# Performance work log

Measured on AMD Instinct MI355X. Metric: run time of the kernel, lower is better.

## Reference

```python
import jax, jax.numpy as jnp
import numpy as np

B, NE, NS, NI, NIS, H, NL = 8192, 210, 7, 8, 2, 128, 3


def setup_inputs() -> dict:
    key = jax.random.key(0)
    ks = jax.random.split(key, 24)
    inp = {}
    inp["F_dist"] = jax.random.normal(ks[0], (B, 45), jnp.float32)
    inp["F_cos"] = jax.random.normal(ks[1], (B, NE), jnp.float32)
    inp["F_sin"] = jax.random.normal(ks[2], (B, NE), jnp.float32)
    inp["F_angle"] = jax.random.normal(ks[3], (B, 8), jnp.float32)
    # Zscore tables: row 0 = mean, row 1 = std (kept away from zero)
    def zscore(k, f):
        k1, k2 = jax.random.split(k)
        mean = jax.random.normal(k1, (1, f), jnp.float32)
        std = jax.random.uniform(k2, (1, f), jnp.float32, 0.5, 1.5)
        return jnp.concatenate([mean, std], axis=0)
    inp["Zscore_dist"] = zscore(ks[4], 45)
    inp["Zscore_cos"] = zscore(ks[5], NE)
    inp["Zscore_sin"] = zscore(ks[6], NE)
    # per-expert index tables
    inp["INDEX3_4BD"] = jax.random.randint(ks[7], (NE, 6), 0, 45, jnp.int32)
    inp["INDEX5"] = jax.random.randint(ks[8], (NS,), 0, NE, jnp.int32)
    # 210 experts: Linear(8,H) + (NL-1)x Linear(H,H) + Linear(H,1), all tanh-separated
    s = 0.1
    inp["W1"] = jax.random.normal(ks[9], (NE, NI, H), jnp.float32) * s
    inp["b1"] = jax.random.normal(ks[10], (NE, H), jnp.float32) * s
    inp["Wh"] = jax.random.normal(ks[11], (NL - 1, NE, H, H), jnp.float32) * s
    inp["bh"] = jax.random.normal(ks[12], (NL - 1, NE, H), jnp.float32) * s
    inp["Wo"] = jax.random.normal(ks[13], (NE, H, 1), jnp.float32) * s
    inp["bo"] = jax.random.normal(ks[14], (NE, 1), jnp.float32) * s
    # 7 small experts: Linear(2,H) + (NL-1)x Linear(H,H) + Linear(H,1)
    inp["W1s"] = jax.random.normal(ks[15], (NS, NIS, H), jnp.float32) * s
    inp["b1s"] = jax.random.normal(ks[16], (NS, H), jnp.float32) * s
    inp["Whs"] = jax.random.normal(ks[17], (NL - 1, NS, H, H), jnp.float32) * s
    inp["bhs"] = jax.random.normal(ks[18], (NL - 1, NS, H), jnp.float32) * s
    inp["Wos"] = jax.random.normal(ks[19], (NS, H, 1), jnp.float32) * s
    inp["bos"] = jax.random.normal(ks[20], (NS, 1), jnp.float32) * s
    return inp


def _expert_stack(F, W1, b1, Wh, bh, Wo, bo):
    # F: [B, E, ni] -> [B, E, 1]; grouped tiny MLPs with tanh
    h = jnp.tanh(jnp.einsum("bei,eih->beh", F, W1) + b1)
    for l in range(Wh.shape[0]):
        h = jnp.tanh(jnp.einsum("beh,ehg->beg", h, Wh[l]) + bh[l])
    return jnp.einsum("beh,eho->beo", h, Wo) + bo


def reference(F_dist, F_cos, F_sin, F_angle, Zscore_dist, Zscore_cos, Zscore_sin,
              INDEX3_4BD, INDEX5,
              W1, b1, Wh, bh, Wo, bo, W1s, b1s, Whs, bhs, Wos, bos):
    FNorm_dist = (F_dist - Zscore_dist[0]) / Zscore_dist[1]  # [B,45]
    FNorm_cos = (F_cos - Zscore_cos[0]) / Zscore_cos[1]      # [B,210]
    FNorm_sin = (F_sin - Zscore_sin[0]) / Zscore_sin[1]      # [B,210]
    # gather per-expert 6 dist features + own cos/sin -> [B,210,8]
    Fd = FNorm_dist[:, INDEX3_4BD]                            # [B,210,6]
    F = jnp.concatenate([Fd, FNorm_cos[:, :, None], FNorm_sin[:, :, None]], axis=-1)
    out = _expert_stack(F, W1, b1, Wh, bh, Wo, bo)            # [B,210,1]
    total = jnp.sum(out, axis=1)                              # [B,1]
    # 7 small experts on (cos, sin) pairs picked by INDEX5
    Fs = jnp.stack([FNorm_cos[:, INDEX5], FNorm_sin[:, INDEX5]], axis=-1)  # [B,7,2]
    outs = _expert_stack(Fs, W1s, b1s, Whs, bhs, Wos, bos)    # [B,7,1]
    total = total + jnp.sum(outs, axis=1)
    return total
```

## Files before the change

### kernel.cpp

```cpp
#include <hip/hip_runtime.h>
#include <hip/hip_bf16.h>
#include <stdint.h>

#define NB 8192
#define NE 210
#define NS 7
#define NEXP 217
#define NI 8
#define H 128
#define BT 256
#define NTILE (NB / BT)
#define BLOB_STRIDE 71680
#define BIAS_OFF 4096
#define WH0_OFF 6144
#define WH1_OFF 38912
#define SMEM_BYTES 67584

#define O_BLOB 0u
#define O_F    16000000u
#define O_FS   43525120u
#define O_PART 43754496u

typedef __attribute__((ext_vector_type(8))) short bf16x8;
typedef __attribute__((ext_vector_type(4))) float f32x4;
typedef __attribute__((ext_vector_type(16))) float f32x16;
typedef __attribute__((ext_vector_type(2))) int i32x2;

union I4V { int4 i; bf16x8 v; unsigned u[4]; };
union C16 { f32x16 v; f32x4 q[4]; };

__device__ __forceinline__ unsigned short f2bf(float f) {
  unsigned u = __float_as_uint(f);
  u += 0x7fffu + ((u >> 16) & 1u);
  return (unsigned short)(u >> 16);
}
__device__ __forceinline__ float fast_tanh(float x) {
  float e = __builtin_amdgcn_exp2f(2.8853900817779268f * x);
  return 1.0f - 2.0f * __builtin_amdgcn_rcpf(1.0f + e);
}
__device__ __forceinline__ unsigned pk_bf16(float a, float b) {
  unsigned r;
  asm("v_cvt_pk_bf16_f32 %0, %1, %2" : "=v"(r) : "v"(a), "v"(b));
  return r;
}
__device__ __forceinline__ void glds16(const void* g, void* l) {
  __builtin_amdgcn_global_load_lds(
      (const __attribute__((address_space(1))) unsigned int*)g,
      (__attribute__((address_space(3))) unsigned int*)l, 16, 0, 0);
}

__device__ __forceinline__ void transition(const f32x16 (&acc)[4], bf16x8 (&bn)[8]) {
#pragma unroll
  for (int kk = 0; kk < 8; ++kk) {
    const int ms = kk >> 1, ko = (kk & 1) * 8;
    unsigned P0 = pk_bf16(fast_tanh(acc[ms][ko + 0]), fast_tanh(acc[ms][ko + 1]));
    unsigned P1 = pk_bf16(fast_tanh(acc[ms][ko + 2]), fast_tanh(acc[ms][ko + 3]));
    unsigned P2 = pk_bf16(fast_tanh(acc[ms][ko + 4]), fast_tanh(acc[ms][ko + 5]));
    unsigned P3 = pk_bf16(fast_tanh(acc[ms][ko + 6]), fast_tanh(acc[ms][ko + 7]));
    i32x2 s0 = __builtin_amdgcn_permlane32_swap((int)P0, (int)P2, false, false);
    i32x2 s1 = __builtin_amdgcn_permlane32_swap((int)P1, (int)P3, false, false);
    I4V r;
    r.u[0] = (unsigned)s0.x;
    r.u[1] = (unsigned)s1.x;
    r.u[2] = (unsigned)s0.y;
    r.u[3] = (unsigned)s1.y;
    bn[kk] = r.v;
  }
}

__device__ __forceinline__ void hidden_layer(f32x16 (&acc)[4], const bf16x8 (&bn)[8],
                                             const uint8_t* wb, const float* biaL,
                                             int row, int hi, int hi4) {
  {
    int soff0 = (hi ^ (row & 15)) << 4;
#pragma unroll
    for (int mt = 0; mt < 4; ++mt) {
      bf16x8 aF = *(const bf16x8*)(wb + (mt * 32 + row) * 256 + soff0);
      C16 c0;
#pragma unroll
      for (int i = 0; i < 4; ++i)
        c0.q[i] = *(const f32x4*)(biaL + mt * 32 + i * 8 + hi4);
      acc[mt] = __builtin_amdgcn_mfma_f32_32x32x16_bf16(aF, bn[0], c0.v, 0, 0, 0);
    }
  }
#pragma unroll
  for (int kk = 1; kk < 8; ++kk) {
    int soff = ((2 * kk + hi) ^ (row & 15)) << 4;
#pragma unroll
    for (int mt = 0; mt < 4; ++mt) {
      bf16x8 aF = *(const bf16x8*)(wb + (mt * 32 + row) * 256 + soff);
      acc[mt] = __builtin_amdgcn_mfma_f32_32x32x16_bf16(aF, bn[kk], acc[mt], 0, 0, 0);
    }
  }
}

__global__ __launch_bounds__(128) void k_pack(
    const float* __restrict__ W1, const float* __restrict__ Wh,
    const float* __restrict__ W1s, const float* __restrict__ Whs,
    const float* __restrict__ bh, const float* __restrict__ bhs,
    const float* __restrict__ Wo, const float* __restrict__ Wos,
    const float* __restrict__ bo, const float* __restrict__ bos,
    uint8_t* __restrict__ blob) {
  int bid = blockIdx.x;
  int e = bid / 3, sec = bid % 3;
  int n = threadIdx.x;
  uint8_t* be = blob + (size_t)e * BLOB_STRIDE;
  bool big = e < NE;
  int s = e - NE;
  if (sec == 0) {
    union { int4 v[2]; unsigned short u[16]; } row;
    row.v[0] = make_int4(0, 0, 0, 0);
    row.v[1] = make_int4(0, 0, 0, 0);
    if (big) {
      for (int k = 0; k < NI; ++k) row.u[k] = f2bf(W1[((size_t)e * NI + k) * H + n]);
    } else {
      for (int k = 0; k < 2; ++k) row.u[k] = f2bf(W1s[((size_t)s * 2 + k) * H + n]);
    }
    *(int4*)(be + n * 32) = row.v[0];
    *(int4*)(be + n * 32 + 16) = row.v[1];
    float* bsec = (float*)(be + BIAS_OFF);
    bsec[n]       = big ? bh[(size_t)e * H + n]          : bhs[(size_t)s * H + n];
    bsec[128 + n] = big ? bh[((size_t)NE + e) * H + n]   : bhs[((size_t)NS + s) * H + n];
    bsec[256 + n] = big ? Wo[(size_t)e * H + n]          : Wos[(size_t)s * H + n];
    if (n == 0) bsec[384] = big ? bo[e] : bos[s];
  } else {
    int l = sec - 1;
    union { int4 v[16]; unsigned short u[128]; } row;
    if (big) {
      for (int k = 0; k < H; ++k)
        row.u[k] = f2bf(Wh[(((size_t)l * NE + e) * H + k) * H + n]);
    } else {
      for (int k = 0; k < H; ++k)
        row.u[k] = f2bf(Whs[(((size_t)l * NS + s) * H + k) * H + n]);
    }
    int4* dst = (int4*)(be + (l ? WH1_OFF : WH0_OFF) + n * 256);
    for (int c = 0; c < 16; ++c) dst[c] = row.v[c ^ (n & 15)];
  }
}

__global__ __launch_bounds__(256) void k_fbuild(
    const float* __restrict__ F_dist, const float* __restrict__ F_cos,
    const float* __restrict__ F_sin,
    const float* __restrict__ Zd, const float* __restrict__ Zc,
    const float* __restrict__ Zs,
    const int* __restrict__ IDX3, const int* __restrict__ IDX5,
    uint16_t* __restrict__ F, uint16_t* __restrict__ Fs) {
  int bid = blockIdx.x;
  int e = bid >> 5, tile = bid & 31;
  int b = tile * 256 + threadIdx.x;
  if (e < NE) {
    float cv = (F_cos[(size_t)b * NE + e] - Zc[e]) / Zc[NE + e];
    float sv = (F_sin[(size_t)b * NE + e] - Zs[e]) / Zs[NE + e];
    union { int4 v; unsigned short u[8]; } o;
    for (int j = 0; j < 6; ++j) {
      int id = IDX3[e * 6 + j];
      float x = (F_dist[(size_t)b * 45 + id] - Zd[id]) / Zd[45 + id];
      o.u[j] = f2bf(x);
    }
    o.u[6] = f2bf(cv);
    o.u[7] = f2bf(sv);
    *(int4*)(F + ((size_t)e * NB + b) * 8) = o.v;
  } else {
    int s = e - NE;
    int id = IDX5[s];
    float cv = (F_cos[(size_t)b * NE + id] - Zc[id]) / Zc[NE + id];
    float sv = (F_sin[(size_t)b * NE + id] - Zs[id]) / Zs[NE + id];
    unsigned o = (unsigned)f2bf(cv) | ((unsigned)f2bf(sv) << 16);
    *(unsigned*)(Fs + ((size_t)s * NB + b) * 2) = o;
  }
}

__global__ __launch_bounds__(512, 4) void k_main(
    const uint8_t* __restrict__ blob,
    const uint16_t* __restrict__ F, const uint16_t* __restrict__ Fs,
    const float* __restrict__ b1, const float* __restrict__ b1s,
    float* __restrict__ partial) {
  extern __shared__ __attribute__((aligned(16))) uint8_t smem[];

  int bid = blockIdx.x;
  const int TOT = NEXP * NTILE;
  int lb = (bid & 7) * (TOT >> 3) + (bid >> 3);
  int e = lb >> 5;
  int tile = lb & 31;
  int brow = tile * BT;

  int t = threadIdx.x;
  int w = t >> 6, lane = t & 63;
  int row = lane & 31, hi = lane >> 5;
  int hi4 = hi << 2;

  bool big = e < NE;
  int s = e - NE;
  const uint8_t* be = blob + (size_t)e * BLOB_STRIDE;

  I4V bfr;
  bfr.i = make_int4(0, 0, 0, 0);
  if (hi == 0) {
    if (big) {
      bfr.i = *(const int4*)(F + ((size_t)e * NB + brow + w * 32 + row) * 8);
    } else {
      bfr.u[0] = *(const unsigned*)(Fs + ((size_t)s * NB + brow + w * 32 + row) * 2);
    }
  }
  const float* bias1 = big ? b1 + (size_t)e * H : b1s + (size_t)s * H;
  I4V aW[4];
  C16 c1[4];
#pragma unroll
  for (int mt = 0; mt < 4; ++mt) {
    aW[mt].i = *(const int4*)(be + (mt * 32 + row) * 32 + hi * 16);
#pragma unroll
    for (int i = 0; i < 4; ++i)
      c1[mt].q[i] = *(const f32x4*)(bias1 + mt * 32 + i * 8 + hi4);
  }
  __builtin_amdgcn_sched_barrier(0);

  for (int c = w; c < 34; c += 8)
    glds16(be + BIAS_OFF + c * 1024 + lane * 16, smem + c * 1024);
  __builtin_amdgcn_sched_barrier(0);
  for (int c = 34 + w; c < 66; c += 8)
    glds16(be + BIAS_OFF + c * 1024 + lane * 16, smem + c * 1024);
  __builtin_amdgcn_sched_barrier(0);

  f32x16 acc[4];
#pragma unroll
  for (int mt = 0; mt < 4; ++mt)
    acc[mt] = __builtin_amdgcn_mfma_f32_32x32x16_bf16(aW[mt].v, bfr.v, c1[mt].v, 0, 0, 0);

  bf16x8 bn[8];
  transition(acc, bn);

  asm volatile("s_waitcnt vmcnt(4)" ::: "memory");
  __builtin_amdgcn_s_barrier();
  __builtin_amdgcn_sched_barrier(0);

  hidden_layer(acc, bn, smem + 2048, (const float*)smem, row, hi, hi4);
  transition(acc, bn);

  asm volatile("s_waitcnt vmcnt(0)" ::: "memory");
  __builtin_amdgcn_s_barrier();
  __builtin_amdgcn_sched_barrier(0);

  hidden_layer(acc, bn, smem + 34816, (const float*)(smem + 512), row, hi, hi4);

  {
    const float* woL = (const float*)(smem + 1024);
    float bout = *(const float*)(smem + 1536);
    float sum = 0.f;
#pragma unroll
    for (int mt = 0; mt < 4; ++mt)
#pragma unroll
      for (int i = 0; i < 4; ++i) {
        f32x4 wq = *(const f32x4*)(woL + mt * 32 + i * 8 + hi4);
#pragma unroll
        for (int j = 0; j < 4; ++j)
          sum += fast_tanh(acc[mt][4 * i + j]) * wq[j];
      }
    sum += __shfl_xor(sum, 32);
    if (hi == 0)
      partial[(size_t)e * NB + brow + w * 32 + row] = sum + bout;
  }
}

__global__ __launch_bounds__(256) void k_reduce(const float* __restrict__ partial,
                                                float* __restrict__ out) {
  int b = blockIdx.x * 256 + threadIdx.x;
  float s = 0.f;
  for (int e = 0; e < NEXP; ++e) s += partial[(size_t)e * NB + b];
  out[b] = s;
}

extern "C" void kernel_launch(void* const* d_in, const int* in_sizes, int n_in,
                              void* d_out, int out_size, void* d_ws, size_t ws_size,
                              hipStream_t stream) {
  const float* F_dist = (const float*)d_in[0];
  const float* F_cos  = (const float*)d_in[1];
  const float* F_sin  = (const float*)d_in[2];
  const float* Zd  = (const float*)d_in[4];
  const float* Zc  = (const float*)d_in[5];
  const float* Zs  = (const float*)d_in[6];
  const int* IDX3  = (const int*)d_in[7];
  const int* IDX5  = (const int*)d_in[8];
  const float* W1  = (const float*)d_in[9];
  const float* b1  = (const float*)d_in[10];
  const float* Wh  = (const float*)d_in[11];
  const float* bh  = (const float*)d_in[12];
  const float* Wo  = (const float*)d_in[13];
  const float* bo  = (const float*)d_in[14];
  const float* W1s = (const float*)d_in[15];
  const float* b1s = (const float*)d_in[16];
  const float* Whs = (const float*)d_in[17];
  const float* bhs = (const float*)d_in[18];
  const float* Wos = (const float*)d_in[19];
  const float* bos = (const float*)d_in[20];

  uint8_t* ws = (uint8_t*)d_ws;
  uint8_t* blob = ws + O_BLOB;
  uint16_t* F   = (uint16_t*)(ws + O_F);
  uint16_t* Fs  = (uint16_t*)(ws + O_FS);
  float* partial = (float*)(ws + O_PART);

  hipFuncSetAttribute(reinterpret_cast<const void*>(k_main),
                      hipFuncAttributeMaxDynamicSharedMemorySize, SMEM_BYTES);

  k_pack<<<NEXP * 3, 128, 0, stream>>>(W1, Wh, W1s, Whs, bh, bhs, Wo, Wos, bo, bos, blob);
  k_fbuild<<<NEXP * 32, 256, 0, stream>>>(F_dist, F_cos, F_sin, Zd, Zc, Zs,
                                          IDX3, IDX5, F, Fs);
  k_main<<<NEXP * NTILE, 512, SMEM_BYTES, stream>>>(blob, F, Fs, b1, b1s, partial);
  k_reduce<<<NB / 256, 256, 0, stream>>>(partial, (float*)d_out);
}
```

Measured before the change: 270.4 us.

## Process two 256-row batch groups per block to reuse staged expert weights

Doubles the batch tile per block to 512 rows, so each block runs the expert MLP twice (two 256-row groups) with the same LDS-staged hidden-layer weights. This halves the number of blocks and the repeated global-to-LDS weight loads per expert. The second group's inputs and first-layer weights are reloaded after the first group's hidden layers, with asm barriers keeping the compiler from hoisting them. The cost is longer serial work per block, fewer blocks for latency hiding, and possibly more register pressure.

```diff
diff --git a/kernel.cpp b/kernel.cpp
--- a/kernel.cpp
+++ b/kernel.cpp
@@ -8,7 +8,7 @@
 #define NEXP 217
 #define NI 8
 #define H 128
-#define BT 256
+#define BT 512
 #define NTILE (NB / BT)
 #define BLOB_STRIDE 71680
 #define BIAS_OFF 4096
@@ -92,6 +92,36 @@
       acc[mt] = __builtin_amdgcn_mfma_f32_32x32x16_bf16(aF, bn[kk], acc[mt], 0, 0, 0);
     }
   }
+}
+
+__device__ __forceinline__ void run_group(
+    const I4V (&aW)[4], const C16 (&c1)[4], const I4V& bfr,
+    const uint8_t* smem, float* __restrict__ partial,
+    size_t pbase, int row, int hi, int hi4) {
+  f32x16 acc[4];
+#pragma unroll
+  for (int mt = 0; mt < 4; ++mt)
+    acc[mt] = __builtin_amdgcn_mfma_f32_32x32x16_bf16(aW[mt].v, bfr.v, c1[mt].v, 0, 0, 0);
+  bf16x8 bn[8];
+  transition(acc, bn);
+  hidden_layer(acc, bn, smem + 2048, (const float*)smem, row, hi, hi4);
+  transition(acc, bn);
+  hidden_layer(acc, bn, smem + 34816, (const float*)(smem + 512), row, hi, hi4);
+  const float* woL = (const float*)(smem + 1024);
+  float bout = *(const float*)(smem + 1536);
+  float sum = 0.f;
+#pragma unroll
+  for (int mt = 0; mt < 4; ++mt)
+#pragma unroll
+    for (int i = 0; i < 4; ++i) {
+      f32x4 wq = *(const f32x4*)(woL + mt * 32 + i * 8 + hi4);
+#pragma unroll
+      for (int j = 0; j < 4; ++j)
+        sum += fast_tanh(acc[mt][4 * i + j]) * wq[j];
+    }
+  sum += __shfl_xor(sum, 32);
+  if (hi == 0)
+    partial[pbase] = sum + bout;
 }
 
 __global__ __launch_bounds__(128) void k_pack(
@@ -180,8 +210,8 @@
   int bid = blockIdx.x;
   const int TOT = NEXP * NTILE;
   int lb = (bid & 7) * (TOT >> 3) + (bid >> 3);
-  int e = lb >> 5;
-  int tile = lb & 31;
+  int e = lb >> 4;
+  int tile = lb & 15;
   int brow = tile * BT;
 
   int t = threadIdx.x;
@@ -192,15 +222,14 @@
   bool big = e < NE;
   int s = e - NE;
   const uint8_t* be = blob + (size_t)e * BLOB_STRIDE;
-
-  I4V bfr;
-  bfr.i = make_int4(0, 0, 0, 0);
+  size_t fbase = big ? ((size_t)e * NB + brow + w * 32 + row)
+                     : ((size_t)s * NB + brow + w * 32 + row);
+
+  I4V bfr0;
+  bfr0.i = make_int4(0, 0, 0, 0);
   if (hi == 0) {
-    if (big) {
-      bfr.i = *(const int4*)(F + ((size_t)e * NB + brow + w * 32 + row) * 8);
-    } else {
-      bfr.u[0] = *(const unsigned*)(Fs + ((size_t)s * NB + brow + w * 32 + row) * 2);
-    }
+    if (big) bfr0.i = *(const int4*)(F + fbase * 8);
+    else     bfr0.u[0] = *(const unsigned*)(Fs + fbase * 2);
   }
   const float* bias1 = big ? b1 + (size_t)e * H : b1s + (size_t)s * H;
   I4V aW[4];
@@ -224,8 +253,7 @@
   f32x16 acc[4];
 #pragma unroll
   for (int mt = 0; mt < 4; ++mt)
-    acc[mt] = __builtin_amdgcn_mfma_f32_32x32x16_bf16(aW[mt].v, bfr.v, c1[mt].v, 0, 0, 0);
-
+    acc[mt] = __builtin_amdgcn_mfma_f32_32x32x16_bf16(aW[mt].v, bfr0.v, c1[mt].v, 0, 0, 0);
   bf16x8 bn[8];
   transition(acc, bn);
 
@@ -241,6 +269,25 @@
   __builtin_amdgcn_sched_barrier(0);
 
   hidden_layer(acc, bn, smem + 34816, (const float*)(smem + 512), row, hi, hi4);
+
+  const uint8_t* be2 = be;
+  asm("" : "+v"(be2));
+  const float* bias1b = bias1;
+  asm("" : "+v"(bias1b));
+  I4V bfr1, aW2[4];
+  C16 c12[4];
+  bfr1.i = make_int4(0, 0, 0, 0);
+  if (hi == 0) {
+    if (big) bfr1.i = *(const int4*)(F + (fbase + 256) * 8);
+    else     bfr1.u[0] = *(const unsigned*)(Fs + (fbase + 256) * 2);
+  }
+#pragma unroll
+  for (int mt = 0; mt < 4; ++mt) {
+    aW2[mt].i = *(const int4*)(be2 + (mt * 32 + row) * 32 + hi * 16);
+#pragma unroll
+    for (int i = 0; i < 4; ++i)
+      c12[mt].q[i] = *(const f32x4*)(bias1b + mt * 32 + i * 8 + hi4);
+  }
 
   {
     const float* woL = (const float*)(smem + 1024);
@@ -259,6 +306,9 @@
     if (hi == 0)
       partial[(size_t)e * NB + brow + w * 32 + row] = sum + bout;
   }
+
+  run_group(aW2, c12, bfr1, smem, partial,
+            (size_t)e * NB + brow + 256 + w * 32 + row, row, hi, hi4);
 }
 
 __global__ __launch_bounds__(256) void k_reduce(const float* __restrict__ partial,
```

After: 272.7 us. Within noise of the previous version (+0.8%).
